# Kernel optimization log

Measured on AMD Instinct MI355X. Metric: run time of the kernel, lower is better.

The kernel has to match this reference:

```python
import jax, jax.numpy as jnp
import numpy as np

K = 16  # top-k neighbors (init kwarg k)
EPS = 1e-8


def setup_inputs() -> dict:
    key = jax.random.key(0)
    # bs=8, closeness=12, flows=2, N=2048
    x_c = jax.random.normal(key, (8, 12, 2, 2048), dtype=jnp.float32)
    return {"x_c": x_c, "flow": 0}


def _cosine_adjacency(x):
    # x: (bs, 2, N, closeness) -> per-node feature = concat of both flows over time
    bs, f, N, c = x.shape
    feats = jnp.transpose(x, (0, 2, 1, 3)).reshape(bs, N, f * c)  # (bs, N, 2*closeness)
    fn = feats / (jnp.linalg.norm(feats, axis=-1, keepdims=True) + EPS)
    return jnp.einsum('bnd,bmd->bnm', fn, fn)  # (bs, N, N)


def reference(x_c, flow):
    # x_c: (bs, closeness, 2, N)
    bs, closeness, _, N = x_c.shape
    x = jnp.transpose(x_c, (0, 2, 3, 1)).astype(jnp.float32)  # (bs, 2, N, closeness)

    # mode == 'cos': cosine-similarity adjacency
    A = _cosine_adjacency(x)

    # index = argsort(A, descending)[:, :, :k]  ==  top-k neighbor indices per node
    _, index = jax.lax.top_k(A, K)  # (bs, N, K)

    # batched gather replacing the bs x N python double loop:
    # sx_c[i, j] = x[i, flow, index[i, j]]
    x_flow = x[:, flow]  # (bs, N, closeness)
    sx_c = jax.vmap(lambda xf, idx: xf[idx])(x_flow, index)  # (bs, N, K, closeness)

    # tgt_mode == 'c': tgt = x[:, flow].unsqueeze(-2)  -> (bs, N, 1, closeness)
    tgt = x_flow[:, :, None, :]
    # returned as tgt.permute(0,2,3,1).squeeze(1) -> (bs, closeness, N)
    tgt_out = jnp.squeeze(jnp.transpose(tgt, (0, 2, 3, 1)), axis=1)

    return sx_c, tgt_out
```

## Files before the change

### kernel.cpp

```cpp
#include <hip/hip_runtime.h>
#include <hip/hip_bf16.h>
#include <math.h>

#define BS   8
#define NPTS 2048
#define CCH  12
#define NF   2
#define DIM  24
#define KPAD 32
#define KTOP 16
#define NWV  8
#define RPB  16
#define CBUF 112
#define CBS  113
#define WVS  20

#define NROWS    (BS * NPTS)
#define TGT_BASE (NROWS * KTOP * CCH)

typedef unsigned long long u64;
typedef unsigned int       u32;
typedef unsigned short     u16;
typedef __attribute__((ext_vector_type(8))) short short8;
typedef __attribute__((ext_vector_type(4))) float f32x4;

#define WS_FEATS 0
#define WS_RAW   (NROWS * DIM * 4)
#define WS_FHI   (WS_RAW + NROWS * CCH * 4)
#define WS_FLO   (WS_FHI + NROWS * KPAD * 2)

__device__ __forceinline__ float np_norm_den(const float* __restrict__ v)
{
#pragma clang fp contract(off)
    float s[DIM];
    #pragma unroll
    for (int d = 0; d < DIM; ++d) s[d] = v[d] * v[d];
    float r[8];
    #pragma unroll
    for (int j = 0; j < 8; ++j) r[j] = (s[j] + s[j + 8]) + s[j + 16];
    float res = ((r[0] + r[1]) + (r[2] + r[3])) + ((r[4] + r[5]) + (r[6] + r[7]));
    return sqrtf(res) + 1e-8f;
}

__device__ __forceinline__ u32 ordf(float f)
{
    u32 u = __float_as_uint(f);
    return ((int)u >= 0) ? (u | 0x80000000u) : ~u;
}

__device__ __forceinline__ u16 bf16_rne(float x)
{
    u32 bits = __float_as_uint(x);
    bits += 0x7fffu + ((bits >> 16) & 1u);
    return (u16)(bits >> 16);
}

__global__ __launch_bounds__(256) void prep_kernel(
    const float* __restrict__ x_c,
    const int*   __restrict__ flow_p,
    float*       __restrict__ feats,
    u16*         __restrict__ fhi,
    u16*         __restrict__ flo,
    float*       __restrict__ raw,
    float*       __restrict__ out)
{
    const int t = blockIdx.x * 256 + threadIdx.x;
    const int b = t >> 11;
    const int n = t & (NPTS - 1);
    const float* xb = x_c + (size_t)b * CCH * NF * NPTS;

    float v[DIM];
    float fn[DIM];
    {
#pragma clang fp contract(off)
        #pragma unroll
        for (int c = 0; c < CCH; ++c)
            #pragma unroll
            for (int f = 0; f < NF; ++f)
                v[f * CCH + c] = xb[(c * NF + f) * NPTS + n];

        const float den = np_norm_den(v);
        float* fo = feats + (size_t)t * DIM;
        #pragma unroll
        for (int d = 0; d < DIM; ++d) { fn[d] = v[d] / den; fo[d] = fn[d]; }
    }

    u16* ho = fhi + (size_t)t * KPAD;
    u16* lo = flo + (size_t)t * KPAD;
    #pragma unroll
    for (int d = 0; d < DIM; ++d) {
        const u16 hb = bf16_rne(fn[d]);
        const float hf = __uint_as_float((u32)hb << 16);
        ho[d] = hb;
        lo[d] = bf16_rne(fn[d] - hf);
    }
    #pragma unroll
    for (int d = DIM; d < KPAD; ++d) { ho[d] = 0; lo[d] = 0; }

    const int flow = flow_p[0];
    float* ro = raw + (size_t)t * CCH;
    #pragma unroll
    for (int c = 0; c < CCH; ++c) {
        const float xv = flow ? v[CCH + c] : v[c];
        ro[c] = xv;
        out[TGT_BASE + ((size_t)b * CCH + c) * NPTS + n] = xv;
    }
}

#define CLEANUP_DESC(arr)                                         \
    _Pragma("unroll")                                             \
    for (int j_ = 8; j_ > 0; j_ >>= 1)                            \
        _Pragma("unroll")                                         \
        for (int i_ = 0; i_ < KTOP; ++i_) {                       \
            const int l_ = i_ | j_;                               \
            if (l_ > i_) {                                        \
                const float a_ = arr[i_], c_ = arr[l_];           \
                arr[i_] = fmaxf(a_, c_);                          \
                arr[l_] = fminf(a_, c_);                          \
            }                                                     \
        }

__global__ __launch_bounds__(512) void fused_topk_kernel(
    const float* __restrict__ feats,
    const u16*   __restrict__ fhi,
    const u16*   __restrict__ flo,
    const float* __restrict__ raw,
    float*       __restrict__ out)
{
    __shared__ union {
        float wval[NWV * 16 * WVS];
        float vk[NWV * KTOP * 16];
        u64   ckey[RPB * CBS];
    } sh;
    __shared__ float thr_s[RPB];
    __shared__ int   cnt[RPB];
    __shared__ int   sel[RPB][KTOP];

    const int tid  = threadIdx.x;
    const int lane = tid & 63;
    const int w    = __builtin_amdgcn_readfirstlane(tid >> 6);
    const int b     = blockIdx.x >> 7;
    const int chunk = blockIdx.x & 127;
    const int rb    = chunk * RPB;
    const int p     = lane & 15;
    const int q     = lane >> 4;

    if (tid < RPB) cnt[tid] = 0;

    short8 ahi, alo;
    {
        const size_t ae = ((size_t)(b * NPTS + rb + p)) * KPAD + q * 8;
        ahi = *(const short8*)(fhi + ae);
        alo = *(const short8*)(flo + ae);
    }

    float* wv = sh.wval + w * (16 * WVS);

    float vlist[KTOP];
    #pragma unroll
    for (int k = 0; k < KTOP; ++k) vlist[k] = -3.0f;

    for (int ro = 0; ro < 2; ++ro) {
        float bv[16];
        #pragma unroll
        for (int t = 0; t < 4; ++t) {
            const int cb0 = w * 128 + ro * 64 + t * 16;
            const size_t be = ((size_t)(b * NPTS + cb0 + p)) * KPAD + q * 8;
            const short8 bhi = *(const short8*)(fhi + be);
            const short8 blo = *(const short8*)(flo + be);
            f32x4 acc = {0.0f, 0.0f, 0.0f, 0.0f};
            acc = __builtin_amdgcn_mfma_f32_16x16x32_bf16(ahi, bhi, acc, 0, 0, 0);
            acc = __builtin_amdgcn_mfma_f32_16x16x32_bf16(ahi, blo, acc, 0, 0, 0);
            acc = __builtin_amdgcn_mfma_f32_16x16x32_bf16(alo, bhi, acc, 0, 0, 0);
            *(f32x4*)(wv + p * WVS + q * 4) = acc;
            #pragma unroll
            for (int i = 0; i < 4; ++i)
                bv[t * 4 + i] = wv[(q * 4 + i) * WVS + p];
        }
        #pragma unroll
        for (int k = 2; k <= 16; k <<= 1)
            #pragma unroll
            for (int j = k >> 1; j > 0; j >>= 1)
                #pragma unroll
                for (int i = 0; i < 16; ++i) {
                    const int l = i | j;
                    if (l > i) {
                        const float a = bv[i], c = bv[l];
                        if ((i & k) == 0) { bv[i] = fminf(a, c); bv[l] = fmaxf(a, c); }
                        else              { bv[i] = fmaxf(a, c); bv[l] = fminf(a, c); }
                    }
                }
        #pragma unroll
        for (int i = 0; i < 16; ++i) vlist[i] = fmaxf(vlist[i], bv[i]);
        CLEANUP_DESC(vlist)
    }

    #pragma unroll
    for (int x = 16; x <= 32; x <<= 1) {
        float other[KTOP];
        #pragma unroll
        for (int k = 0; k < KTOP; ++k) other[k] = __shfl_xor(vlist[k], x);
        #pragma unroll
        for (int i = 0; i < KTOP; ++i)
            vlist[i] = fmaxf(vlist[i], other[KTOP - 1 - i]);
        CLEANUP_DESC(vlist)
    }

    __syncthreads();

    for (int half = NWV / 2; half >= 1; half >>= 1) {
        if (w >= half && w < 2 * half && q == 0) {
            #pragma unroll
            for (int k = 0; k < KTOP; ++k)
                sh.vk[(w * KTOP + k) * 16 + p] = vlist[k];
        }
        __syncthreads();
        if (w < half) {
            float other[KTOP];
            #pragma unroll
            for (int k = 0; k < KTOP; ++k)
                other[k] = sh.vk[((w + half) * KTOP + k) * 16 + p];
            #pragma unroll
            for (int i = 0; i < KTOP; ++i)
                vlist[i] = fmaxf(vlist[i], other[KTOP - 1 - i]);
            CLEANUP_DESC(vlist)
        }
        __syncthreads();
    }
    if (w == 0 && q == 0) thr_s[p] = vlist[KTOP - 1] - 8e-4f;
    __syncthreads();

    float thrv[4];
    #pragma unroll
    for (int i = 0; i < 4; ++i) thrv[i] = thr_s[q * 4 + i];

    {
        size_t be_n = ((size_t)(b * NPTS + w * 256 + p)) * KPAD + q * 8;
        short8 nbhi = *(const short8*)(fhi + be_n);
        short8 nblo = *(const short8*)(flo + be_n);
        for (int t = 0; t < 16; ++t) {
            const int cb0 = w * 256 + t * 16;
            const short8 bhi = nbhi, blo = nblo;
            if (t < 15) {
                const size_t be = ((size_t)(b * NPTS + cb0 + 16 + p)) * KPAD + q * 8;
                nbhi = *(const short8*)(fhi + be);
                nblo = *(const short8*)(flo + be);
            }
            f32x4 acc = {0.0f, 0.0f, 0.0f, 0.0f};
            acc = __builtin_amdgcn_mfma_f32_16x16x32_bf16(ahi, bhi, acc, 0, 0, 0);
            acc = __builtin_amdgcn_mfma_f32_16x16x32_bf16(ahi, blo, acc, 0, 0, 0);
            acc = __builtin_amdgcn_mfma_f32_16x16x32_bf16(alo, bhi, acc, 0, 0, 0);
            #pragma unroll
            for (int i = 0; i < 4; ++i) {
                if (acc[i] >= thrv[i]) {
                    const int r = q * 4 + i;
                    const int pos = atomicAdd(&cnt[r], 1);
                    if (pos < CBUF)
                        sh.ckey[r * CBS + pos] = (u64)(u32)(cb0 + p);
                }
            }
        }
    }
    __syncthreads();

    {
        const int r = tid & 15;
        const float* fr = feats + (size_t)(b * NPTS + rb + r) * DIM;
        float rfn[DIM];
        #pragma unroll
        for (int d = 0; d < DIM; ++d) rfn[d] = fr[d];
        const int e = (cnt[r] < CBUF) ? cnt[r] : CBUF;
        for (int pos = tid >> 4; pos < e; pos += 32) {
            const int idx = (int)(u32)sh.ckey[r * CBS + pos];
            const float* cp = feats + (size_t)(b * NPTS + idx) * DIM;
            float acc = 0.0f;
            #pragma unroll
            for (int d = 0; d < DIM; ++d)
                acc = __builtin_fmaf(cp[d], rfn[d], acc);
            sh.ckey[r * CBS + pos] = ((u64)ordf(acc) << 32) | (u32)(2047 - idx);
        }
    }
    __syncthreads();

    {
        const int L = tid >> 5;
        const int g = tid & 31;
        const int e = (cnt[L] < CBUF) ? cnt[L] : CBUF;
        const u64* rowbuf = &sh.ckey[L * CBS];
        for (int pos = g; pos < e; pos += 32) {
            const u64 key = rowbuf[pos];
            int rank = 0;
            for (int p2 = 0; p2 < e; ++p2) rank += (rowbuf[p2] > key);
            if (rank < KTOP) sel[L][rank] = 2047 - (int)(key & 0xFFFFFFFFull);
        }
    }
    __syncthreads();

    const int rg = b * NPTS + rb;
    for (int e2 = tid; e2 < RPB * KTOP * CCH; e2 += 512) {
        const int L = e2 / (KTOP * CCH);
        const int r = e2 % (KTOP * CCH);
        const int k = r / CCH;
        const int c = r % CCH;
        out[((size_t)(rg + L) * KTOP + k) * CCH + c] =
            raw[((size_t)b * NPTS + sel[L][k]) * CCH + c];
    }
}

extern "C" void kernel_launch(void* const* d_in, const int* in_sizes, int n_in,
                              void* d_out, int out_size, void* d_ws, size_t ws_size,
                              hipStream_t stream)
{
    const float* x_c    = (const float*)d_in[0];
    const int*   flow_p = (const int*)d_in[1];
    float*       out    = (float*)d_out;

    float* feats = (float*)((char*)d_ws + WS_FEATS);
    float* raw   = (float*)((char*)d_ws + WS_RAW);
    u16*   fhi   = (u16*)  ((char*)d_ws + WS_FHI);
    u16*   flo   = (u16*)  ((char*)d_ws + WS_FLO);

    prep_kernel<<<NROWS / 256, 256, 0, stream>>>(x_c, flow_p, feats, fhi, flo, raw, out);
    fused_topk_kernel<<<BS * 128, 512, 0, stream>>>(feats, fhi, flo, raw, out);
}
```

Before: 101.6 us.

## Sample fewer columns for top-k threshold and merge wave lists in one wave

The threshold pre-pass now samples 64 columns per wave instead of 128. Each wave sorts its 16-value list once, with loads software-prefetched, and no longer merges across two rounds. The cross-wave reduction is replaced by one store and a single wave that merges the 8 wave lists via registers and shuffles, which removes several block barriers. The candidate buffer is doubled, since a looser threshold from fewer samples lets more candidates pass and could otherwise overflow.

```diff
diff --git a/kernel.cpp b/kernel.cpp
--- a/kernel.cpp
+++ b/kernel.cpp
@@ -11,8 +11,8 @@
 #define KTOP 16
 #define NWV  8
 #define RPB  16
-#define CBUF 112
-#define CBS  113
+#define CBUF 224
+#define CBS  225
 #define WVS  20
 
 #define NROWS    (BS * NPTS)
@@ -120,6 +120,12 @@
             }                                                     \
         }
 
+#define MERGE_DESC(a, b)                                          \
+    _Pragma("unroll")                                             \
+    for (int i_ = 0; i_ < KTOP; ++i_)                             \
+        a[i_] = fmaxf(a[i_], b[KTOP - 1 - i_]);                   \
+    CLEANUP_DESC(a)
+
 __global__ __launch_bounds__(512) void fused_topk_kernel(
     const float* __restrict__ feats,
     const u16*   __restrict__ fhi,
@@ -157,17 +163,18 @@
     float* wv = sh.wval + w * (16 * WVS);
 
     float vlist[KTOP];
-    #pragma unroll
-    for (int k = 0; k < KTOP; ++k) vlist[k] = -3.0f;
-
-    for (int ro = 0; ro < 2; ++ro) {
-        float bv[16];
+    {
+        size_t be_n = ((size_t)(b * NPTS + w * 64 + p)) * KPAD + q * 8;
+        short8 nbhi = *(const short8*)(fhi + be_n);
+        short8 nblo = *(const short8*)(flo + be_n);
         #pragma unroll
         for (int t = 0; t < 4; ++t) {
-            const int cb0 = w * 128 + ro * 64 + t * 16;
-            const size_t be = ((size_t)(b * NPTS + cb0 + p)) * KPAD + q * 8;
-            const short8 bhi = *(const short8*)(fhi + be);
-            const short8 blo = *(const short8*)(flo + be);
+            const short8 bhi = nbhi, blo = nblo;
+            if (t < 3) {
+                const size_t be = ((size_t)(b * NPTS + w * 64 + (t + 1) * 16 + p)) * KPAD + q * 8;
+                nbhi = *(const short8*)(fhi + be);
+                nblo = *(const short8*)(flo + be);
+            }
             f32x4 acc = {0.0f, 0.0f, 0.0f, 0.0f};
             acc = __builtin_amdgcn_mfma_f32_16x16x32_bf16(ahi, bhi, acc, 0, 0, 0);
             acc = __builtin_amdgcn_mfma_f32_16x16x32_bf16(ahi, blo, acc, 0, 0, 0);
@@ -175,7 +182,7 @@
             *(f32x4*)(wv + p * WVS + q * 4) = acc;
             #pragma unroll
             for (int i = 0; i < 4; ++i)
-                bv[t * 4 + i] = wv[(q * 4 + i) * WVS + p];
+                vlist[t * 4 + i] = wv[(q * 4 + i) * WVS + p];
         }
         #pragma unroll
         for (int k = 2; k <= 16; k <<= 1)
@@ -185,49 +192,48 @@
                 for (int i = 0; i < 16; ++i) {
                     const int l = i | j;
                     if (l > i) {
-                        const float a = bv[i], c = bv[l];
-                        if ((i & k) == 0) { bv[i] = fminf(a, c); bv[l] = fmaxf(a, c); }
-                        else              { bv[i] = fmaxf(a, c); bv[l] = fminf(a, c); }
+                        const float a = vlist[i], c = vlist[l];
+                        if ((i & k) == 0) { vlist[i] = fmaxf(a, c); vlist[l] = fminf(a, c); }
+                        else              { vlist[i] = fminf(a, c); vlist[l] = fmaxf(a, c); }
                     }
                 }
         #pragma unroll
-        for (int i = 0; i < 16; ++i) vlist[i] = fmaxf(vlist[i], bv[i]);
-        CLEANUP_DESC(vlist)
-    }
-
-    #pragma unroll
-    for (int x = 16; x <= 32; x <<= 1) {
-        float other[KTOP];
-        #pragma unroll
-        for (int k = 0; k < KTOP; ++k) other[k] = __shfl_xor(vlist[k], x);
-        #pragma unroll
-        for (int i = 0; i < KTOP; ++i)
-            vlist[i] = fmaxf(vlist[i], other[KTOP - 1 - i]);
-        CLEANUP_DESC(vlist)
-    }
-
-    __syncthreads();
-
-    for (int half = NWV / 2; half >= 1; half >>= 1) {
-        if (w >= half && w < 2 * half && q == 0) {
-            #pragma unroll
-            for (int k = 0; k < KTOP; ++k)
-                sh.vk[(w * KTOP + k) * 16 + p] = vlist[k];
-        }
-        __syncthreads();
-        if (w < half) {
+        for (int x = 16; x <= 32; x <<= 1) {
             float other[KTOP];
             #pragma unroll
-            for (int k = 0; k < KTOP; ++k)
-                other[k] = sh.vk[((w + half) * KTOP + k) * 16 + p];
-            #pragma unroll
-            for (int i = 0; i < KTOP; ++i)
-                vlist[i] = fmaxf(vlist[i], other[KTOP - 1 - i]);
-            CLEANUP_DESC(vlist)
-        }
-        __syncthreads();
-    }
-    if (w == 0 && q == 0) thr_s[p] = vlist[KTOP - 1] - 8e-4f;
+            for (int k = 0; k < KTOP; ++k) other[k] = __shfl_xor(vlist[k], x);
+            MERGE_DESC(vlist, other)
+        }
+    }
+
+    __syncthreads();
+
+    if (q == 0) {
+        #pragma unroll
+        for (int k = 0; k < KTOP; ++k)
+            sh.vk[(w * KTOP + k) * 16 + p] = vlist[k];
+    }
+    __syncthreads();
+
+    if (w == 0) {
+        const int r = lane >> 2;
+        const int g = lane & 3;
+        float va[KTOP], vb[KTOP];
+        #pragma unroll
+        for (int k = 0; k < KTOP; ++k) {
+            va[k] = sh.vk[((2 * g) * KTOP + k) * 16 + r];
+            vb[k] = sh.vk[((2 * g + 1) * KTOP + k) * 16 + r];
+        }
+        MERGE_DESC(va, vb)
+        #pragma unroll
+        for (int x = 1; x <= 2; x <<= 1) {
+            float other[KTOP];
+            #pragma unroll
+            for (int k = 0; k < KTOP; ++k) other[k] = __shfl_xor(va[k], x);
+            MERGE_DESC(va, other)
+        }
+        if (g == 0) thr_s[r] = va[KTOP - 1] - 8e-4f;
+    }
     __syncthreads();
 
     float thrv[4];
```

After: 112.4 us. 10.6% more time.
